# Kernel optimization log

Hardware: AMD Instinct MI355X
Metric: run time of the kernel (lower is better)

## Reference

```python
import jax, jax.numpy as jnp
import numpy as np

B, S, H = 2, 2048, 4096
NH, HD = 32, 128          # heads, head_dim = H // NH
ROPE_THETA = 10000.0
CLIP_QKV = 8.0
SCALE = HD ** -0.5


def setup_inputs() -> dict:
    key = jax.random.key(0)
    k1, k2, k3 = jax.random.split(key, 3)
    hidden_states = jax.random.normal(k1, (B, S, H), dtype=jnp.float32)
    positions = jnp.arange(S, dtype=jnp.int32)
    # 0.02 init scale keeps qkv magnitudes realistic so the +/-8 clamp rarely saturates
    w_qkv = jax.random.normal(k2, (3 * H, H), dtype=jnp.float32) * 0.02
    w_o = jax.random.normal(k3, (H, H), dtype=jnp.float32) * 0.02
    return {"hidden_states": hidden_states, "positions": positions,
            "w_qkv": w_qkv, "w_o": w_o}


def _rope(x, positions):
    # x: [B, S, NH, HD]; neox-style rotary over full head_dim
    half = HD // 2
    inv_freq = 1.0 / (ROPE_THETA ** (jnp.arange(0, half, dtype=jnp.float32) / half))
    ang = positions.astype(jnp.float32)[:, None] * inv_freq[None, :]  # [S, half]
    cos = jnp.cos(ang)[None, :, None, :]
    sin = jnp.sin(ang)[None, :, None, :]
    x1, x2 = x[..., :half], x[..., half:]
    return jnp.concatenate([x1 * cos - x2 * sin, x2 * cos + x1 * sin], axis=-1)


def reference(hidden_states, positions, w_qkv, w_o):
    # fused QKV projection (no bias) + clamp
    qkv = jnp.einsum('bsh,oh->bso', hidden_states, w_qkv)
    qkv = jnp.clip(qkv, -CLIP_QKV, CLIP_QKV)
    q, k, v = jnp.split(qkv, 3, axis=-1)            # each [B, S, H]
    q = q.reshape(B, S, NH, HD)
    k = k.reshape(B, S, NH, HD)
    v = v.reshape(B, S, NH, HD)
    q = _rope(q, positions)
    k = _rope(k, positions)
    # causal attention
    scores = jnp.einsum('bqhd,bkhd->bhqk', q, k) * SCALE
    causal = jnp.tril(jnp.ones((S, S), dtype=bool))
    scores = jnp.where(causal[None, None], scores, jnp.finfo(scores.dtype).min)
    probs = jax.nn.softmax(scores, axis=-1)
    attn = jnp.einsum('bhqk,bkhd->bqhd', probs, v).reshape(B, S, H)
    return jnp.einsum('bsh,oh->bso', attn, w_o)
```

## Files before the change

kernel.cpp:

```cpp
#include <hip/hip_runtime.h>
#include <hip/hip_bf16.h>

#define BATCH 2
#define SEQ 2048
#define HID 4096
#define NHEAD 32
#define HDIM 128
#define BH (BATCH*NHEAD)
#define MROWS (BATCH*SEQ)
#define ATT_SCALE 0.08838834764831845f

typedef __attribute__((ext_vector_type(8))) short bf16x8;
typedef __attribute__((ext_vector_type(4))) float f32x4;

__device__ __forceinline__ float bf2f(short x){
  union { float f; unsigned u; } v; v.u = ((unsigned)(unsigned short)x) << 16; return v.f;
}
__device__ __forceinline__ short f2bf(float f){
  union { float f; unsigned u; } v; v.f = f;
  unsigned r = v.u + 0x7fffu + ((v.u >> 16) & 1u);
  return (short)(r >> 16);
}
__device__ __forceinline__ void gload_lds16(const void* g, void* l){
  __builtin_amdgcn_global_load_lds(
    (const __attribute__((address_space(1))) void*)g,
    (__attribute__((address_space(3))) void*)l, 16, 0, 0);
}

__global__ void cvt_bf16(const float* __restrict__ in, short* __restrict__ out, int n4){
  int i = blockIdx.x*blockDim.x + threadIdx.x;
  int stride = gridDim.x*blockDim.x;
  for (; i < n4; i += stride){
    float4 v = ((const float4*)in)[i];
    short4 o;
    o.x = f2bf(v.x); o.y = f2bf(v.y); o.z = f2bf(v.z); o.w = f2bf(v.w);
    ((short4*)out)[i] = o;
  }
}

__global__ void rope_table_k(const int* __restrict__ pos, float* __restrict__ tab){
  int idx = blockIdx.x*blockDim.x + threadIdx.x;
  if (idx >= SEQ*64) return;
  int s = idx >> 6, d = idx & 63;
  float p = (float)pos[s];
  float inv = exp2f(-(float)d * (13.287712379549449f/64.0f));
  float ang = p * inv;
  tab[2*idx]   = cosf(ang);
  tab[2*idx+1] = sinf(ang);
}

template<int W>
__device__ __forceinline__ void stage_half(const short* __restrict__ gsrc, int ldg,
                                           short* lds, int tid, int h){
  #pragma unroll
  for (int li=0; li<2; ++li){
    int e16 = li*512 + tid;
    int rs = e16 >> 3, ck = e16 & 7;
    int r = ((rs/W)*2 + h)*W + (rs%W);
    gload_lds16(gsrc + (size_t)r*ldg + ((ck ^ (r&7))<<3),
                lds + r*64 + ck*8);
  }
}

__device__ __forceinline__ void load_afrags(const short* Asb, int wr, int c, int g,
                                            int Mh, bf16x8 (&afr)[4][2]){
  #pragma unroll
  for (int mi=0; mi<4; ++mi){
    int row = wr*128 + (Mh*4+mi)*16 + c;
    const char* bp = (const char*)Asb + row*128;
    #pragma unroll
    for (int kk=0; kk<2; ++kk)
      afr[mi][kk] = *(const bf16x8*)(bp + ((kk*64 + g*16) ^ ((row&7)<<4)));
  }
}
__device__ __forceinline__ void load_bfrags(const short* Bsb, int wc, int c, int g,
                                            int Nh, bf16x8 (&bfr)[2][2]){
  #pragma unroll
  for (int ni=0; ni<2; ++ni){
    int row = wc*64 + (Nh*2+ni)*16 + c;
    const char* bp = (const char*)Bsb + row*128;
    #pragma unroll
    for (int kk=0; kk<2; ++kk)
      bfr[ni][kk] = *(const bf16x8*)(bp + ((kk*64 + g*16) ^ ((row&7)<<4)));
  }
}
template<int MH, int NH>
__device__ __forceinline__ void mma_quad(bf16x8 (&afr)[4][2], bf16x8 (&bfr)[2][2],
                                         f32x4 (&acc)[8][4]){
  #pragma unroll
  for (int kk=0; kk<2; ++kk)
    #pragma unroll
    for (int mi=0; mi<4; ++mi)
      #pragma unroll
      for (int ni=0; ni<2; ++ni)
        acc[MH*4+mi][NH*2+ni] = __builtin_amdgcn_mfma_f32_16x16x32_bf16(
            afr[mi][kk], bfr[ni][kk], acc[MH*4+mi][NH*2+ni], 0,0,0);
}

#define BAR()  asm volatile("s_barrier" ::: "memory")
#define VMC4() asm volatile("s_waitcnt vmcnt(4)" ::: "memory")
#define VMC0() asm volatile("s_waitcnt vmcnt(0)" ::: "memory")

#define PHASE(BUF, MH, NH, DO_A, DO_B, STAGE_STMT, VM_STMT)              \
  {                                                                      \
    if (DO_A) load_afrags(&As[BUF][0], wr, c, g, MH, afr);               \
    if (DO_B) load_bfrags(&Bs[BUF][0], wc, c, g, NH, bfr);               \
    STAGE_STMT;                                                          \
    if (DO_A && DO_B) asm volatile("s_waitcnt lgkmcnt(8)" ::: "memory"); \
    BAR();                                                               \
    asm volatile("s_waitcnt lgkmcnt(0)" ::: "memory");                   \
    __builtin_amdgcn_s_setprio(1);                                       \
    mma_quad<MH,NH>(afr, bfr, acc);                                      \
    __builtin_amdgcn_s_setprio(0);                                       \
    VM_STMT;                                                             \
    BAR();                                                               \
  }

template<int MODE>
__global__ __launch_bounds__(512, 2) void gemm8p(
    const short* __restrict__ A, const short* __restrict__ Bw,
    short* __restrict__ Qb, short* __restrict__ Kb, short* __restrict__ Vb,
    float* __restrict__ Of){
  __shared__ __align__(16) short As[2][256*64];
  __shared__ __align__(16) short Bs[2][256*64];
  const int K = HID;
  int tid = threadIdx.x, lane = tid & 63, w = tid >> 6;
  int wr = w >> 2, wc = w & 3, g = lane >> 4, c = lane & 15;
  int gx = gridDim.x;
  int nwg = gx * gridDim.y;
  int bid = blockIdx.y*gx + blockIdx.x;
  int cpx = nwg >> 3;
  int swz = (bid & 7)*cpx + (bid >> 3);
  int m0 = (swz / gx) * 256, n0 = (swz % gx) * 256;

  const short* Abase = A  + (size_t)m0*K;
  const short* Bbase = Bw + (size_t)n0*K;
  auto stageA = [&](int buf, int kt, int h){
    stage_half<64>(Abase + kt*64, K, &As[buf][0], tid, h);
  };
  auto stageB = [&](int buf, int kt, int h){
    stage_half<32>(Bbase + kt*64, K, &Bs[buf][0], tid, h);
  };

  f32x4 acc[8][4];
  f32x4 zero = {0.f,0.f,0.f,0.f};
  #pragma unroll
  for (int i=0;i<8;++i)
    #pragma unroll
    for (int j=0;j<4;++j) acc[i][j] = zero;
  bf16x8 afr[4][2], bfr[2][2];

  stageA(0, 0, 0); stageA(0, 0, 1);
  stageB(0, 0, 0); stageB(0, 0, 1);
  stageB(1, 1, 0); stageA(1, 1, 1);
  VMC4();
  BAR();

  const int NITER = K/128;
  for (int i = 0; i < NITER-1; ++i){
    int t1 = 2*i+1, t2 = 2*i+2, t3 = 2*i+3;
    PHASE(0, 0,0, true,  true,  stageA(1, t1, 0), (void)0)
    PHASE(0, 1,0, true,  false, stageB(1, t1, 1), (void)0)
    PHASE(0, 1,1, false, true,  stageB(0, t2, 0), (void)0)
    PHASE(0, 0,1, true,  false, stageA(0, t2, 1), VMC4())
    PHASE(1, 0,0, true,  true,  stageA(0, t2, 0), (void)0)
    PHASE(1, 1,0, true,  false, stageB(0, t2, 1), (void)0)
    PHASE(1, 1,1, false, true,  stageB(1, t3, 0), (void)0)
    PHASE(1, 0,1, true,  false, stageA(1, t3, 1), VMC4())
  }
  {
    int t1 = 2*(NITER-1)+1;
    PHASE(0, 0,0, true,  true,  stageA(1, t1, 0), (void)0)
    PHASE(0, 1,0, true,  false, stageB(1, t1, 1), (void)0)
    PHASE(0, 1,1, false, true,  (void)0,          (void)0)
    PHASE(0, 0,1, true,  false, (void)0,          VMC0())
    PHASE(1, 0,0, true,  true,  (void)0,          (void)0)
    PHASE(1, 1,0, true,  false, (void)0,          (void)0)
    PHASE(1, 1,1, false, true,  (void)0,          (void)0)
    PHASE(1, 0,1, true,  false, (void)0,          (void)0)
  }

  #pragma unroll
  for (int fa=0; fa<8; ++fa){
    #pragma unroll
    for (int fb=0; fb<4; ++fb){
      f32x4 v = acc[fa][fb];
      #pragma unroll
      for (int rr=0; rr<4; ++rr){
        int row = m0 + wr*128 + fa*16 + g*4 + rr;
        int col = n0 + wc*64  + fb*16 + c;
        float x = v[rr];
        if (MODE == 0){
          x = fminf(fmaxf(x, -8.0f), 8.0f);
          int sel = col >> 12, wi = col & 4095;
          int head = wi >> 7, d = wi & 127;
          int b = row >> 11, s = row & 2047;
          size_t off = ((size_t)(b*NHEAD + head)*SEQ + s)*HDIM + d;
          short* dst = (sel == 0) ? Qb : (sel == 1) ? Kb : Vb;
          dst[off] = f2bf(x);
        } else {
          Of[(size_t)row*HID + col] = x;
        }
      }
    }
  }
}

__global__ void rope_apply_k(short* __restrict__ Qb, short* __restrict__ Kb,
                             const float* __restrict__ tab){
  int idx = blockIdx.x*blockDim.x + threadIdx.x;
  if (idx >= BH*SEQ*64) return;
  int d = idx & 63;
  int s = (idx >> 6) & (SEQ-1);
  int bh = idx >> 17;
  size_t base = ((size_t)bh*SEQ + s)*HDIM;
  float cs = tab[2*(s*64+d)], sn = tab[2*(s*64+d)+1];
  float q1 = bf2f(Qb[base+d]), q2 = bf2f(Qb[base+d+64]);
  Qb[base+d]    = f2bf(q1*cs - q2*sn);
  Qb[base+d+64] = f2bf(q2*cs + q1*sn);
  float k1 = bf2f(Kb[base+d]), k2 = bf2f(Kb[base+d+64]);
  Kb[base+d]    = f2bf(k1*cs - k2*sn);
  Kb[base+d+64] = f2bf(k2*cs + k1*sn);
}

__global__ void transpose_v_k(const short* __restrict__ V, short* __restrict__ Vt){
  __shared__ short t[32][33];
  int bh = blockIdx.z;
  int s0 = blockIdx.x*32, d0 = blockIdx.y*32;
  int tx = threadIdx.x & 31, ty = threadIdx.x >> 5;
  const short* src = V + ((size_t)bh*SEQ + s0)*HDIM + d0;
  #pragma unroll
  for (int i=ty;i<32;i+=8) t[i][tx] = src[(size_t)i*HDIM + tx];
  __syncthreads();
  short* dst = Vt + ((size_t)bh*HDIM + d0)*SEQ + s0;
  #pragma unroll
  for (int i=ty;i<32;i+=8) dst[(size_t)i*SEQ + tx] = t[tx][i];
}

__global__ __launch_bounds__(256) void flash_attn_k(
    const short* __restrict__ Qb, const short* __restrict__ Kb,
    const short* __restrict__ Vt, short* __restrict__ attn){
  __shared__ short Ks[2][64*128];
  __shared__ short Vs[2][128*64];
  __shared__ short Ps[4][16][72];
  int tid = threadIdx.x, lane = tid & 63, w = tid >> 6;
  int g = lane >> 4, c = lane & 15;
  int flat = blockIdx.y*gridDim.x + blockIdx.x;
  int xcd = flat & 7, idx = flat >> 3;
  int bh = xcd + 8*(idx >> 5);
  int qblk = idx & 31;
  int q0 = qblk * 64;
  int qw = q0 + w*16;
  bf16x8 qf[4];
  #pragma unroll
  for (int ks=0;ks<4;++ks)
    qf[ks] = *(const bf16x8*)(Qb + ((size_t)bh*SEQ + qw + c)*HDIM + ks*32 + g*8);
  f32x4 o[8];
  f32x4 zero = {0.f,0.f,0.f,0.f};
  #pragma unroll
  for (int i=0;i<8;++i) o[i] = zero;
  float m_r[4] = {-1e30f,-1e30f,-1e30f,-1e30f};
  float l_r[4] = {0.f,0.f,0.f,0.f};

  auto stage = [&](int j, int b){
    int kv0 = j*64;
    #pragma unroll
    for (int i=0;i<4;++i){
      int e = i*256 + tid;
      int kr = e >> 4, kc = e & 15;
      gload_lds16(Kb + ((size_t)bh*SEQ + kv0 + kr)*HDIM + (size_t)((kc ^ (kr&7))*8),
                  &Ks[b][kr*128 + kc*8]);
      int vr = e >> 3, vc = e & 7;
      gload_lds16(Vt + ((size_t)bh*HDIM + vr)*SEQ + kv0 + (size_t)((vc ^ (vr&7))*8),
                  &Vs[b][vr*64 + vc*8]);
    }
  };

  stage(0, 0);
  __syncthreads();
  int buf = 0;
  for (int j=0;j<=qblk;++j){
    if (j < qblk) stage(j+1, buf^1);

    int kv0 = j*64;
    f32x4 sf[4];
    #pragma unroll
    for (int fj=0;fj<4;++fj) sf[fj] = zero;
    __builtin_amdgcn_s_setprio(1);
    #pragma unroll
    for (int ks=0;ks<4;++ks){
      #pragma unroll
      for (int fj=0;fj<4;++fj){
        int kvrow = fj*16 + c;
        bf16x8 kb = *(const bf16x8*)&Ks[buf][kvrow*128 + (((ks*4+g) ^ (c&7))*8)];
        sf[fj] = __builtin_amdgcn_mfma_f32_16x16x32_bf16(qf[ks], kb, sf[fj], 0,0,0);
      }
    }
    __builtin_amdgcn_s_setprio(0);
    bool diag = (j == qblk);
    float rmax[4];
    #pragma unroll
    for (int rr=0;rr<4;++rr){
      #pragma unroll
      for (int fj=0;fj<4;++fj){
        float v = sf[fj][rr] * ATT_SCALE;
        if (diag && (kv0 + fj*16 + c) > (qw + g*4 + rr)) v = -1e30f;
        sf[fj][rr] = v;
      }
      float t = fmaxf(fmaxf(sf[0][rr], sf[1][rr]), fmaxf(sf[2][rr], sf[3][rr]));
      t = fmaxf(t, __shfl_xor(t, 1));
      t = fmaxf(t, __shfl_xor(t, 2));
      t = fmaxf(t, __shfl_xor(t, 4));
      t = fmaxf(t, __shfl_xor(t, 8));
      rmax[rr] = t;
    }
    float alpha[4];
    #pragma unroll
    for (int rr=0;rr<4;++rr){
      float mnew = fmaxf(m_r[rr], rmax[rr]);
      alpha[rr] = __expf(m_r[rr] - mnew);
      m_r[rr] = mnew;
      float ps = 0.f;
      #pragma unroll
      for (int fj=0;fj<4;++fj){
        float p = __expf(sf[fj][rr] - mnew);
        sf[fj][rr] = p;
        ps += p;
      }
      ps += __shfl_xor(ps, 1);
      ps += __shfl_xor(ps, 2);
      ps += __shfl_xor(ps, 4);
      ps += __shfl_xor(ps, 8);
      l_r[rr] = l_r[rr]*alpha[rr] + ps;
    }
    #pragma unroll
    for (int ni=0;ni<8;++ni){
      f32x4 t = o[ni];
      t[0]*=alpha[0]; t[1]*=alpha[1]; t[2]*=alpha[2]; t[3]*=alpha[3];
      o[ni] = t;
    }
    #pragma unroll
    for (int fj=0;fj<4;++fj)
      #pragma unroll
      for (int rr=0;rr<4;++rr)
        Ps[w][g*4+rr][fj*16+c] = f2bf(sf[fj][rr]);
    __builtin_amdgcn_s_setprio(1);
    #pragma unroll
    for (int ks=0;ks<2;++ks){
      bf16x8 pa = *(const bf16x8*)&Ps[w][c][ks*32 + g*8];
      #pragma unroll
      for (int ni=0;ni<8;++ni){
        int d = ni*16 + c;
        bf16x8 vb = *(const bf16x8*)&Vs[buf][d*64 + (((ks*4+g) ^ (c&7))*8)];
        o[ni] = __builtin_amdgcn_mfma_f32_16x16x32_bf16(pa, vb, o[ni], 0,0,0);
      }
    }
    __builtin_amdgcn_s_setprio(0);
    __syncthreads();
    buf ^= 1;
  }
  int b = bh >> 5, h = bh & 31;
  #pragma unroll
  for (int rr=0;rr<4;++rr){
    float inv = 1.0f / l_r[rr];
    int s = qw + g*4 + rr;
    #pragma unroll
    for (int ni=0;ni<8;++ni){
      int d = ni*16 + c;
      attn[((size_t)(b*SEQ + s))*HID + h*HDIM + d] = f2bf(o[ni][rr] * inv);
    }
  }
}

extern "C" void kernel_launch(void* const* d_in, const int* in_sizes, int n_in,
                              void* d_out, int out_size, void* d_ws, size_t ws_size,
                              hipStream_t stream){
  const float* hs   = (const float*)d_in[0];
  const int*   pos  = (const int*)d_in[1];
  const float* wqkv = (const float*)d_in[2];
  const float* wo   = (const float*)d_in[3];
  float* out = (float*)d_out;
  char* ws = (char*)d_ws;
  size_t off = 0;
  auto alloc = [&](size_t bytes){ void* p = ws + off; off += (bytes + 255) & ~(size_t)255; return p; };
  short* hsb   = (short*)alloc((size_t)MROWS*HID*2);
  short* wqkvb = (short*)alloc((size_t)3*HID*HID*2);
  short* wob   = (short*)alloc((size_t)HID*HID*2);
  short* Qb    = (short*)alloc((size_t)BH*SEQ*HDIM*2);
  short* Kb    = (short*)alloc((size_t)BH*SEQ*HDIM*2);
  short* Vb    = (short*)alloc((size_t)BH*SEQ*HDIM*2);
  short* Vt    = (short*)alloc((size_t)BH*SEQ*HDIM*2);
  short* attn  = (short*)alloc((size_t)MROWS*HID*2);
  float* tab   = (float*)alloc((size_t)SEQ*64*2*4);
  (void)ws_size; (void)in_sizes; (void)n_in; (void)out_size;

  cvt_bf16<<<1024,256,0,stream>>>(hs,   hsb,   MROWS*HID/4);
  cvt_bf16<<<2048,256,0,stream>>>(wqkv, wqkvb, 3*HID*HID/4);
  cvt_bf16<<<1024,256,0,stream>>>(wo,   wob,   HID*HID/4);
  rope_table_k<<<(SEQ*64+255)/256,256,0,stream>>>(pos, tab);
  gemm8p<0><<<dim3(48,16),512,0,stream>>>(hsb, wqkvb, Qb, Kb, Vb, nullptr);
  rope_apply_k<<<(BH*SEQ*64+255)/256,256,0,stream>>>(Qb, Kb, tab);
  transpose_v_k<<<dim3(SEQ/32, HDIM/32, BH),256,0,stream>>>(Vb, Vt);
  flash_attn_k<<<dim3(SEQ/64, BH),256,0,stream>>>(Qb, Kb, Vt, attn);
  gemm8p<1><<<dim3(16,16),512,0,stream>>>(attn, wob, nullptr, nullptr, nullptr, out);
}
```

Measured before the change: 856.8 us.

## Replace 8-phase ping-pong GEMM schedule with simple double-buffered loop

Swaps the hand-scheduled eight-phase GEMM pipeline, which interleaved half-tile staging, fragment loads and barriers with partial vmcnt waits, for a plain double-buffered loop. Each k-tile now prefetches the next whole tile, loads all B fragments once plus two halves of A, runs the MFMAs, then waits on everything and issues one barrier. The aim is fewer barriers and simpler code, at the cost of less fine-grained overlap between global loads, LDS reads and MFMA work.

```diff
diff --git a/kernel.cpp b/kernel.cpp
--- a/kernel.cpp
+++ b/kernel.cpp
@@ -49,6 +49,7 @@
   tab[2*idx+1] = sinf(ang);
 }
 
+
 template<int W>
 __device__ __forceinline__ void stage_half(const short* __restrict__ gsrc, int ldg,
                                            short* lds, int tid, int h){
@@ -62,8 +63,19 @@
   }
 }
 
-__device__ __forceinline__ void load_afrags(const short* Asb, int wr, int c, int g,
-                                            int Mh, bf16x8 (&afr)[4][2]){
+__device__ __forceinline__ void read_bfrags(const short* Bsb, int wc, int c, int g,
+                                            bf16x8 (&bfr)[4][2]){
+  #pragma unroll
+  for (int ni=0; ni<4; ++ni){
+    int row = wc*64 + ni*16 + c;
+    const char* bp = (const char*)Bsb + row*128;
+    #pragma unroll
+    for (int kk=0; kk<2; ++kk)
+      bfr[ni][kk] = *(const bf16x8*)(bp + ((kk*64 + g*16) ^ ((row&7)<<4)));
+  }
+}
+__device__ __forceinline__ void read_ahalf(const short* Asb, int wr, int c, int g,
+                                           int Mh, bf16x8 (&afr)[4][2]){
   #pragma unroll
   for (int mi=0; mi<4; ++mi){
     int row = wr*128 + (Mh*4+mi)*16 + c;
@@ -73,51 +85,25 @@
       afr[mi][kk] = *(const bf16x8*)(bp + ((kk*64 + g*16) ^ ((row&7)<<4)));
   }
 }
-__device__ __forceinline__ void load_bfrags(const short* Bsb, int wc, int c, int g,
-                                            int Nh, bf16x8 (&bfr)[2][2]){
-  #pragma unroll
-  for (int ni=0; ni<2; ++ni){
-    int row = wc*64 + (Nh*2+ni)*16 + c;
-    const char* bp = (const char*)Bsb + row*128;
-    #pragma unroll
-    for (int kk=0; kk<2; ++kk)
-      bfr[ni][kk] = *(const bf16x8*)(bp + ((kk*64 + g*16) ^ ((row&7)<<4)));
-  }
-}
-template<int MH, int NH>
-__device__ __forceinline__ void mma_quad(bf16x8 (&afr)[4][2], bf16x8 (&bfr)[2][2],
-                                         f32x4 (&acc)[8][4]){
+template<int MH>
+__device__ __forceinline__ void mfma_half(bf16x8 (&afr)[4][2], bf16x8 (&bfr)[4][2],
+                                          f32x4 (&acc)[8][4]){
   #pragma unroll
   for (int kk=0; kk<2; ++kk)
     #pragma unroll
     for (int mi=0; mi<4; ++mi)
       #pragma unroll
-      for (int ni=0; ni<2; ++ni)
-        acc[MH*4+mi][NH*2+ni] = __builtin_amdgcn_mfma_f32_16x16x32_bf16(
-            afr[mi][kk], bfr[ni][kk], acc[MH*4+mi][NH*2+ni], 0,0,0);
+      for (int ni=0; ni<4; ++ni)
+        acc[MH*4+mi][ni] = __builtin_amdgcn_mfma_f32_16x16x32_bf16(
+            afr[mi][kk], bfr[ni][kk], acc[MH*4+mi][ni], 0,0,0);
 }
 
 #define BAR()  asm volatile("s_barrier" ::: "memory")
-#define VMC4() asm volatile("s_waitcnt vmcnt(4)" ::: "memory")
 #define VMC0() asm volatile("s_waitcnt vmcnt(0)" ::: "memory")
-
-#define PHASE(BUF, MH, NH, DO_A, DO_B, STAGE_STMT, VM_STMT)              \
-  {                                                                      \
-    if (DO_A) load_afrags(&As[BUF][0], wr, c, g, MH, afr);               \
-    if (DO_B) load_bfrags(&Bs[BUF][0], wc, c, g, NH, bfr);               \
-    STAGE_STMT;                                                          \
-    if (DO_A && DO_B) asm volatile("s_waitcnt lgkmcnt(8)" ::: "memory"); \
-    BAR();                                                               \
-    asm volatile("s_waitcnt lgkmcnt(0)" ::: "memory");                   \
-    __builtin_amdgcn_s_setprio(1);                                       \
-    mma_quad<MH,NH>(afr, bfr, acc);                                      \
-    __builtin_amdgcn_s_setprio(0);                                       \
-    VM_STMT;                                                             \
-    BAR();                                                               \
-  }
+#define LGK0() asm volatile("s_waitcnt lgkmcnt(0)" ::: "memory")
 
 template<int MODE>
-__global__ __launch_bounds__(512, 2) void gemm8p(
+__global__ __launch_bounds__(512, 2) void gemm_rp(
     const short* __restrict__ A, const short* __restrict__ Bw,
     short* __restrict__ Qb, short* __restrict__ Kb, short* __restrict__ Vb,
     float* __restrict__ Of){
@@ -135,11 +121,11 @@
 
   const short* Abase = A  + (size_t)m0*K;
   const short* Bbase = Bw + (size_t)n0*K;
-  auto stageA = [&](int buf, int kt, int h){
-    stage_half<64>(Abase + kt*64, K, &As[buf][0], tid, h);
-  };
-  auto stageB = [&](int buf, int kt, int h){
-    stage_half<32>(Bbase + kt*64, K, &Bs[buf][0], tid, h);
+  auto stage_tile = [&](int buf, int kt){
+    stage_half<64>(Abase + kt*64, K, &As[buf][0], tid, 0);
+    stage_half<64>(Abase + kt*64, K, &As[buf][0], tid, 1);
+    stage_half<32>(Bbase + kt*64, K, &Bs[buf][0], tid, 0);
+    stage_half<32>(Bbase + kt*64, K, &Bs[buf][0], tid, 1);
   };
 
   f32x4 acc[8][4];
@@ -148,36 +134,29 @@
   for (int i=0;i<8;++i)
     #pragma unroll
     for (int j=0;j<4;++j) acc[i][j] = zero;
-  bf16x8 afr[4][2], bfr[2][2];
-
-  stageA(0, 0, 0); stageA(0, 0, 1);
-  stageB(0, 0, 0); stageB(0, 0, 1);
-  stageB(1, 1, 0); stageA(1, 1, 1);
-  VMC4();
+  bf16x8 afr[4][2], bfr[4][2];
+
+  stage_tile(0, 0);
+  VMC0();
   BAR();
 
-  const int NITER = K/128;
-  for (int i = 0; i < NITER-1; ++i){
-    int t1 = 2*i+1, t2 = 2*i+2, t3 = 2*i+3;
-    PHASE(0, 0,0, true,  true,  stageA(1, t1, 0), (void)0)
-    PHASE(0, 1,0, true,  false, stageB(1, t1, 1), (void)0)
-    PHASE(0, 1,1, false, true,  stageB(0, t2, 0), (void)0)
-    PHASE(0, 0,1, true,  false, stageA(0, t2, 1), VMC4())
-    PHASE(1, 0,0, true,  true,  stageA(0, t2, 0), (void)0)
-    PHASE(1, 1,0, true,  false, stageB(0, t2, 1), (void)0)
-    PHASE(1, 1,1, false, true,  stageB(1, t3, 0), (void)0)
-    PHASE(1, 0,1, true,  false, stageA(1, t3, 1), VMC4())
-  }
-  {
-    int t1 = 2*(NITER-1)+1;
-    PHASE(0, 0,0, true,  true,  stageA(1, t1, 0), (void)0)
-    PHASE(0, 1,0, true,  false, stageB(1, t1, 1), (void)0)
-    PHASE(0, 1,1, false, true,  (void)0,          (void)0)
-    PHASE(0, 0,1, true,  false, (void)0,          VMC0())
-    PHASE(1, 0,0, true,  true,  (void)0,          (void)0)
-    PHASE(1, 1,0, true,  false, (void)0,          (void)0)
-    PHASE(1, 1,1, false, true,  (void)0,          (void)0)
-    PHASE(1, 0,1, true,  false, (void)0,          (void)0)
+  const int NT = K/64;
+  for (int t = 0; t < NT; ++t){
+    const short* Ab = &As[t&1][0];
+    const short* Bb = &Bs[t&1][0];
+    if (t+1 < NT) stage_tile((t+1)&1, t+1);
+    read_bfrags(Bb, wc, c, g, bfr);
+    read_ahalf(Ab, wr, c, g, 0, afr);
+    __builtin_amdgcn_s_setprio(1);
+    mfma_half<0>(afr, bfr, acc);
+    __builtin_amdgcn_s_setprio(0);
+    read_ahalf(Ab, wr, c, g, 1, afr);
+    __builtin_amdgcn_s_setprio(1);
+    mfma_half<1>(afr, bfr, acc);
+    __builtin_amdgcn_s_setprio(0);
+    LGK0();
+    VMC0();
+    BAR();
   }
 
   #pragma unroll
@@ -398,9 +377,9 @@
   cvt_bf16<<<2048,256,0,stream>>>(wqkv, wqkvb, 3*HID*HID/4);
   cvt_bf16<<<1024,256,0,stream>>>(wo,   wob,   HID*HID/4);
   rope_table_k<<<(SEQ*64+255)/256,256,0,stream>>>(pos, tab);
-  gemm8p<0><<<dim3(48,16),512,0,stream>>>(hsb, wqkvb, Qb, Kb, Vb, nullptr);
+  gemm_rp<0><<<dim3(48,16),512,0,stream>>>(hsb, wqkvb, Qb, Kb, Vb, nullptr);
   rope_apply_k<<<(BH*SEQ*64+255)/256,256,0,stream>>>(Qb, Kb, tab);
   transpose_v_k<<<dim3(SEQ/32, HDIM/32, BH),256,0,stream>>>(Vb, Vt);
   flash_attn_k<<<dim3(SEQ/64, BH),256,0,stream>>>(Qb, Kb, Vt, attn);
-  gemm8p<1><<<dim3(16,16),512,0,stream>>>(attn, wob, nullptr, nullptr, nullptr, out);
-}
+  gemm_rp<1><<<dim3(16,16),512,0,stream>>>(attn, wob, nullptr, nullptr, nullptr, out);
+}
```

After: 908.7 us. +6.1%, slower.

## Reschedule GEMM main loop to reuse B fragments across quadrants and reorder staging

Applied to the files above, without the earlier changes.

Replaces the PHASE macro schedule in the bf16 GEMM with a hand-written sequence that keeps two B-fragment register sets so each LDS read of A or B feeds two MFMA quadrants (snake order 00,01,11,10). It reduces LDS fragment reads per k-tile and moves the global-to-LDS staging issues and vmcnt waits (now 6/8 instead of 4). The goal is to cut LDS traffic and better overlap loads with MFMA. The cost is more VGPRs for the extra fragment set and a more fragile buffer-hazard schedule.

```diff
diff --git a/kernel.cpp b/kernel.cpp
--- a/kernel.cpp
+++ b/kernel.cpp
@@ -49,6 +49,7 @@
   tab[2*idx+1] = sinf(ang);
 }
 
+
 template<int W>
 __device__ __forceinline__ void stage_half(const short* __restrict__ gsrc, int ldg,
                                            short* lds, int tid, int h){
@@ -62,8 +63,8 @@
   }
 }
 
-__device__ __forceinline__ void load_afrags(const short* Asb, int wr, int c, int g,
-                                            int Mh, bf16x8 (&afr)[4][2]){
+__device__ __forceinline__ void read_ahalf(const short* Asb, int wr, int c, int g,
+                                           int Mh, bf16x8 (&afr)[4][2]){
   #pragma unroll
   for (int mi=0; mi<4; ++mi){
     int row = wr*128 + (Mh*4+mi)*16 + c;
@@ -73,8 +74,8 @@
       afr[mi][kk] = *(const bf16x8*)(bp + ((kk*64 + g*16) ^ ((row&7)<<4)));
   }
 }
-__device__ __forceinline__ void load_bfrags(const short* Bsb, int wc, int c, int g,
-                                            int Nh, bf16x8 (&bfr)[2][2]){
+__device__ __forceinline__ void read_bhalf(const short* Bsb, int wc, int c, int g,
+                                           int Nh, bf16x8 (&bfr)[2][2]){
   #pragma unroll
   for (int ni=0; ni<2; ++ni){
     int row = wc*64 + (Nh*2+ni)*16 + c;
@@ -84,40 +85,29 @@
       bfr[ni][kk] = *(const bf16x8*)(bp + ((kk*64 + g*16) ^ ((row&7)<<4)));
   }
 }
-template<int MH, int NH>
-__device__ __forceinline__ void mma_quad(bf16x8 (&afr)[4][2], bf16x8 (&bfr)[2][2],
-                                         f32x4 (&acc)[8][4]){
+template<int MH, int NHH>
+__device__ __forceinline__ void mma_q(bf16x8 (&afr)[4][2], bf16x8 (&bfr)[2][2],
+                                      f32x4 (&acc)[8][4]){
   #pragma unroll
   for (int kk=0; kk<2; ++kk)
     #pragma unroll
     for (int mi=0; mi<4; ++mi)
       #pragma unroll
       for (int ni=0; ni<2; ++ni)
-        acc[MH*4+mi][NH*2+ni] = __builtin_amdgcn_mfma_f32_16x16x32_bf16(
-            afr[mi][kk], bfr[ni][kk], acc[MH*4+mi][NH*2+ni], 0,0,0);
+        acc[MH*4+mi][NHH*2+ni] = __builtin_amdgcn_mfma_f32_16x16x32_bf16(
+            afr[mi][kk], bfr[ni][kk], acc[MH*4+mi][NHH*2+ni], 0,0,0);
 }
 
 #define BAR()  asm volatile("s_barrier" ::: "memory")
-#define VMC4() asm volatile("s_waitcnt vmcnt(4)" ::: "memory")
+#define LGK0() asm volatile("s_waitcnt lgkmcnt(0)" ::: "memory")
+#define VMC6() asm volatile("s_waitcnt vmcnt(6)" ::: "memory")
+#define VMC8() asm volatile("s_waitcnt vmcnt(8)" ::: "memory")
 #define VMC0() asm volatile("s_waitcnt vmcnt(0)" ::: "memory")
-
-#define PHASE(BUF, MH, NH, DO_A, DO_B, STAGE_STMT, VM_STMT)              \
-  {                                                                      \
-    if (DO_A) load_afrags(&As[BUF][0], wr, c, g, MH, afr);               \
-    if (DO_B) load_bfrags(&Bs[BUF][0], wc, c, g, NH, bfr);               \
-    STAGE_STMT;                                                          \
-    if (DO_A && DO_B) asm volatile("s_waitcnt lgkmcnt(8)" ::: "memory"); \
-    BAR();                                                               \
-    asm volatile("s_waitcnt lgkmcnt(0)" ::: "memory");                   \
-    __builtin_amdgcn_s_setprio(1);                                       \
-    mma_quad<MH,NH>(afr, bfr, acc);                                      \
-    __builtin_amdgcn_s_setprio(0);                                       \
-    VM_STMT;                                                             \
-    BAR();                                                               \
-  }
+#define SP1()  __builtin_amdgcn_s_setprio(1)
+#define SP0()  __builtin_amdgcn_s_setprio(0)
 
 template<int MODE>
-__global__ __launch_bounds__(512, 2) void gemm8p(
+__global__ __launch_bounds__(512, 2) void gemm8r(
     const short* __restrict__ A, const short* __restrict__ Bw,
     short* __restrict__ Qb, short* __restrict__ Kb, short* __restrict__ Vb,
     float* __restrict__ Of){
@@ -148,36 +138,56 @@
   for (int i=0;i<8;++i)
     #pragma unroll
     for (int j=0;j<4;++j) acc[i][j] = zero;
-  bf16x8 afr[4][2], bfr[2][2];
-
-  stageA(0, 0, 0); stageA(0, 0, 1);
-  stageB(0, 0, 0); stageB(0, 0, 1);
-  stageB(1, 1, 0); stageA(1, 1, 1);
-  VMC4();
+  bf16x8 afr[4][2], bfr0[2][2], bfr1[2][2];
+
+  stageB(0,0,0); stageB(0,0,1); stageA(0,0,0); stageA(0,0,1);
+  stageB(1,1,0); stageB(1,1,1); stageA(1,1,0); stageA(1,1,1);
+  VMC8();
   BAR();
 
   const int NITER = K/128;
   for (int i = 0; i < NITER-1; ++i){
-    int t1 = 2*i+1, t2 = 2*i+2, t3 = 2*i+3;
-    PHASE(0, 0,0, true,  true,  stageA(1, t1, 0), (void)0)
-    PHASE(0, 1,0, true,  false, stageB(1, t1, 1), (void)0)
-    PHASE(0, 1,1, false, true,  stageB(0, t2, 0), (void)0)
-    PHASE(0, 0,1, true,  false, stageA(0, t2, 1), VMC4())
-    PHASE(1, 0,0, true,  true,  stageA(0, t2, 0), (void)0)
-    PHASE(1, 1,0, true,  false, stageB(0, t2, 1), (void)0)
-    PHASE(1, 1,1, false, true,  stageB(1, t3, 0), (void)0)
-    PHASE(1, 0,1, true,  false, stageA(1, t3, 1), VMC4())
+    int t2 = 2*i+2, t3 = 2*i+3;
+    read_ahalf(&As[0][0], wr,c,g, 0, afr);
+    read_bhalf(&Bs[0][0], wc,c,g, 0, bfr0);
+    BAR(); LGK0(); SP1(); mma_q<0,0>(afr,bfr0,acc); SP0(); BAR();
+    read_bhalf(&Bs[0][0], wc,c,g, 1, bfr1);
+    stageB(0, t2, 0);
+    BAR(); LGK0(); SP1(); mma_q<0,1>(afr,bfr1,acc); SP0(); BAR();
+    read_ahalf(&As[0][0], wr,c,g, 1, afr);
+    stageB(0, t2, 1); stageA(0, t2, 0);
+    BAR(); LGK0(); SP1(); mma_q<1,1>(afr,bfr1,acc); SP0(); BAR();
+    BAR(); LGK0(); SP1(); mma_q<1,0>(afr,bfr0,acc); SP0(); VMC6(); BAR();
+    read_ahalf(&As[1][0], wr,c,g, 0, afr);
+    read_bhalf(&Bs[1][0], wc,c,g, 0, bfr0);
+    stageA(0, t2, 1);
+    BAR(); LGK0(); SP1(); mma_q<0,0>(afr,bfr0,acc); SP0(); BAR();
+    read_bhalf(&Bs[1][0], wc,c,g, 1, bfr1);
+    stageB(1, t3, 0);
+    BAR(); LGK0(); SP1(); mma_q<0,1>(afr,bfr1,acc); SP0(); BAR();
+    read_ahalf(&As[1][0], wr,c,g, 1, afr);
+    stageB(1, t3, 1); stageA(1, t3, 0);
+    BAR(); LGK0(); SP1(); mma_q<1,1>(afr,bfr1,acc); SP0(); BAR();
+    stageA(1, t3, 1);
+    BAR(); LGK0(); SP1(); mma_q<1,0>(afr,bfr0,acc); SP0(); VMC8(); BAR();
   }
   {
-    int t1 = 2*(NITER-1)+1;
-    PHASE(0, 0,0, true,  true,  stageA(1, t1, 0), (void)0)
-    PHASE(0, 1,0, true,  false, stageB(1, t1, 1), (void)0)
-    PHASE(0, 1,1, false, true,  (void)0,          (void)0)
-    PHASE(0, 0,1, true,  false, (void)0,          VMC0())
-    PHASE(1, 0,0, true,  true,  (void)0,          (void)0)
-    PHASE(1, 1,0, true,  false, (void)0,          (void)0)
-    PHASE(1, 1,1, false, true,  (void)0,          (void)0)
-    PHASE(1, 0,1, true,  false, (void)0,          (void)0)
+    read_ahalf(&As[0][0], wr,c,g, 0, afr);
+    read_bhalf(&Bs[0][0], wc,c,g, 0, bfr0);
+    BAR(); LGK0(); SP1(); mma_q<0,0>(afr,bfr0,acc); SP0(); BAR();
+    read_bhalf(&Bs[0][0], wc,c,g, 1, bfr1);
+    BAR(); LGK0(); SP1(); mma_q<0,1>(afr,bfr1,acc); SP0(); BAR();
+    read_ahalf(&As[0][0], wr,c,g, 1, afr);
+    BAR(); LGK0(); SP1(); mma_q<1,1>(afr,bfr1,acc); SP0(); BAR();
+    BAR(); LGK0(); SP1(); mma_q<1,0>(afr,bfr0,acc); SP0(); VMC0(); BAR();
+    read_ahalf(&As[1][0], wr,c,g, 0, afr);
+    read_bhalf(&Bs[1][0], wc,c,g, 0, bfr0);
+    BAR(); LGK0(); SP1(); mma_q<0,0>(afr,bfr0,acc); SP0(); BAR();
+    read_bhalf(&Bs[1][0], wc,c,g, 1, bfr1);
+    BAR(); LGK0(); SP1(); mma_q<0,1>(afr,bfr1,acc); SP0(); BAR();
+    read_ahalf(&As[1][0], wr,c,g, 1, afr);
+    BAR(); LGK0(); SP1(); mma_q<1,1>(afr,bfr1,acc); SP0(); BAR();
+    BAR(); LGK0(); SP1(); mma_q<1,0>(afr,bfr0,acc); SP0(); BAR();
   }
 
   #pragma unroll
@@ -398,9 +408,9 @@
   cvt_bf16<<<2048,256,0,stream>>>(wqkv, wqkvb, 3*HID*HID/4);
   cvt_bf16<<<1024,256,0,stream>>>(wo,   wob,   HID*HID/4);
   rope_table_k<<<(SEQ*64+255)/256,256,0,stream>>>(pos, tab);
-  gemm8p<0><<<dim3(48,16),512,0,stream>>>(hsb, wqkvb, Qb, Kb, Vb, nullptr);
+  gemm8r<0><<<dim3(48,16),512,0,stream>>>(hsb, wqkvb, Qb, Kb, Vb, nullptr);
   rope_apply_k<<<(BH*SEQ*64+255)/256,256,0,stream>>>(Qb, Kb, tab);
   transpose_v_k<<<dim3(SEQ/32, HDIM/32, BH),256,0,stream>>>(Vb, Vt);
   flash_attn_k<<<dim3(SEQ/64, BH),256,0,stream>>>(Qb, Kb, Vt, attn);
-  gemm8p<1><<<dim3(16,16),512,0,stream>>>(attn, wob, nullptr, nullptr, nullptr, out);
-}
+  gemm8r<1><<<dim3(16,16),512,0,stream>>>(attn, wob, nullptr, nullptr, nullptr, out);
+}
```

Result: faster. 817.5 us (-4.6%).
